# Kernel optimization log

Measured on AMD Instinct MI355X. Metric: run time of the kernel, lower is better.

The kernel has to match this reference:

```python
import jax, jax.numpy as jnp
import numpy as np

B, S, H = 2, 4096, 1024
WINDOW = 32


def setup_inputs() -> dict:
    key = jax.random.key(0)
    ks = jax.random.split(key, 10)
    s = 1.0 / np.sqrt(H)
    return {
        "hidden_states": jax.random.normal(ks[0], (B, S, H), dtype=jnp.float32),
        "Wq": jax.random.normal(ks[1], (H, H), dtype=jnp.float32) * s,
        "Wk": jax.random.normal(ks[2], (H, H), dtype=jnp.float32) * s,
        "Wv": jax.random.normal(ks[3], (H, H), dtype=jnp.float32) * s,
        "Wo": jax.random.normal(ks[4], (H, H), dtype=jnp.float32) * s,
        "ln_w": jnp.ones((H,), dtype=jnp.float32),
        "ln_b": jnp.zeros((H,), dtype=jnp.float32),
        "W1": jax.random.normal(ks[5], (H // 2, H), dtype=jnp.float32) * s,
        "b1": jnp.zeros((H // 2,), dtype=jnp.float32),
        "W2": jax.random.normal(ks[6], (H, H // 2), dtype=jnp.float32) * (1.0 / np.sqrt(H // 2)),
        "b2": jnp.zeros((H,), dtype=jnp.float32),
    }


def _layernorm(x, w, b, eps=1e-5):
    mu = jnp.mean(x, axis=-1, keepdims=True)
    var = jnp.var(x, axis=-1, keepdims=True)
    return (x - mu) * jax.lax.rsqrt(var + eps) * w + b


def reference(hidden_states, Wq, Wk, Wv, Wo, ln_w, ln_b, W1, b1, W2, b2):
    x = hidden_states  # [B,S,H]
    q = x @ Wq.T
    k = x @ Wk.T
    v = x @ Wv.T
    # banded causal mask: keep j<=i and j >= i-WINDOW+1
    i = jnp.arange(S)[:, None]
    j = jnp.arange(S)[None, :]
    local_mask = (j <= i) & (j >= i - WINDOW + 1)  # [S,S] bool
    scores = jnp.einsum('bqh,bkh->bqk', q, k) / np.sqrt(H)
    scores = jnp.where(local_mask[None], scores, -jnp.inf)
    probs = jax.nn.softmax(scores, axis=-1)
    attn_out = jnp.einsum('bqk,bkh->bqh', probs, v) @ Wo.T
    draft = x + attn_out
    h = _layernorm(draft, ln_w, ln_b)
    h = jax.nn.gelu(h @ W1.T + b1, approximate=False)
    adapter_out = h @ W2.T + b2
    return draft + adapter_out
```

## Files before the change

kernel.cpp:

```cpp
#include <hip/hip_runtime.h>
#include <stdint.h>

typedef unsigned short u16;
typedef __bf16 bfx8 __attribute__((ext_vector_type(8)));
typedef float f32x4 __attribute__((ext_vector_type(4)));

__device__ __forceinline__ u16 f2bf(float x) {
    unsigned int u = __float_as_uint(x);
    u += 0x7fffu + ((u >> 16) & 1u);
    return (u16)(u >> 16);
}
__device__ __forceinline__ float bf2f(u16 v) {
    return __uint_as_float(((unsigned)v) << 16);
}

__device__ __forceinline__ void async16(const void* g, void* l) {
    __builtin_amdgcn_global_load_lds(
        (const __attribute__((address_space(1))) unsigned int*)(uintptr_t)g,
        (__attribute__((address_space(3))) unsigned int*)(unsigned int)(uintptr_t)l,
        16, 0, 0);
}

#define S_BARRIER() asm volatile("s_barrier" ::: "memory")
#define WAIT_VM6() asm volatile("s_waitcnt vmcnt(6)" ::: "memory")
#define WAIT_VM5() asm volatile("s_waitcnt vmcnt(5)" ::: "memory")
#define WAIT_VM2() asm volatile("s_waitcnt vmcnt(2)" ::: "memory")
#define WAIT_VM0() asm volatile("s_waitcnt vmcnt(0)" ::: "memory")

struct CastArgs {
    const float* src[7];
    u16* dst[7];
    int nblk[7];
};
__global__ __launch_bounds__(256) void cast_all(CastArgs a) {
    int b = blockIdx.x, seg = 0;
    while (b >= a.nblk[seg]) { b -= a.nblk[seg]; ++seg; }
    int i = b * 256 + threadIdx.x;
    const float4* p = (const float4*)(a.src[seg] + (size_t)i * 8);
    float4 x = p[0], y = p[1];
    ushort4 o0, o1;
    o0.x = f2bf(x.x); o0.y = f2bf(x.y); o0.z = f2bf(x.z); o0.w = f2bf(x.w);
    o1.x = f2bf(y.x); o1.y = f2bf(y.y); o1.z = f2bf(y.z); o1.w = f2bf(y.w);
    ushort4* q = (ushort4*)(a.dst[seg] + (size_t)i * 8);
    q[0] = o0; q[1] = o1;
}

__global__ __launch_bounds__(512, 2)
void gemm_qkv2(const u16* __restrict__ A, const u16* __restrict__ Bw,
               u16* __restrict__ outq, u16* __restrict__ outk,
               u16* __restrict__ vt, int K) {
    __shared__ __align__(1024) unsigned char lds[131072];
    const int t = threadIdx.x;
    const int lane = t & 63, w = t >> 6;
    const int laneR = lane & 15, laneK = lane >> 4;
    const int wm = w >> 2, wn = w & 3;
    const int b = blockIdx.x;
    const int swz = (b & 7) * 48 + (b >> 3);
    const int row0 = (swz / 12) * 256;
    const int col0 = (swz % 12) * 256;
    const int nt = K >> 6;

    const u16* srcU[4][2];
    unsigned dstU[4][2];
#pragma unroll
    for (int u = 0; u < 4; ++u)
#pragma unroll
        for (int j = 0; j < 2; ++j) {
            int c = ((u & 1) ? 1024 : 0) + j * 512 + t;
            int row = c >> 3;
            int ko = (c & 7) ^ (row & 7);
            if (u < 2) srcU[u][j] = A + (size_t)(row0 + row) * K + ko * 8;
            else       srcU[u][j] = Bw + (size_t)(col0 + row) * K + ko * 8;
            dstU[u][j] = (u >= 2 ? 32768u : 0u) + (unsigned)c * 16u;
        }

#define QSTAGE(U, D, TK)                                                      \
    async16(srcU[U][0] + (TK) * 64, lds + (D) + dstU[U][0]);                  \
    async16(srcU[U][1] + (TK) * 64, lds + (D) + dstU[U][1]);

    f32x4 acc[8][4] = {};
    bfx8 af[4], bf[4];

#define QLDA(D, KS, H)                                                        \
    _Pragma("unroll") for (int m = 0; m < 4; ++m) {                           \
        int r = (H) * 128 + wm * 64 + m * 16 + laneR;                         \
        int ph = ((KS) * 4 + laneK) ^ (r & 7);                                \
        af[m] = *(const bfx8*)(lds + (D) + r * 128 + ph * 16);                \
    }
#define QLDB(D, KS)                                                           \
    _Pragma("unroll") for (int n = 0; n < 4; ++n) {                           \
        int rb = wn * 64 + n * 16 + laneR;                                    \
        int ph = ((KS) * 4 + laneK) ^ (rb & 7);                               \
        bf[n] = *(const bfx8*)(lds + (D) + 32768u + rb * 128 + ph * 16);      \
    }
#define QMFMA(H)                                                              \
    __builtin_amdgcn_s_setprio(1);                                            \
    _Pragma("unroll") for (int m = 0; m < 4; ++m)                             \
        _Pragma("unroll") for (int n = 0; n < 4; ++n)                         \
            acc[(H) * 4 + m][n] = __builtin_amdgcn_mfma_f32_16x16x32_bf16(    \
                af[m], bf[n], acc[(H) * 4 + m][n], 0, 0, 0);                  \
    __builtin_amdgcn_s_setprio(0);

    QSTAGE(0, 0u, 0) QSTAGE(2, 0u, 0) QSTAGE(3, 0u, 0) QSTAGE(1, 0u, 0)
    WAIT_VM2();
    S_BARRIER();

    for (int tk = 0; tk < nt - 1; ++tk) {
        const unsigned d = (unsigned)(tk & 1) * 65536u;
        const unsigned nd = d ^ 65536u;
        const int tn = tk + 1;
        QLDA(d, 0, 0) QLDB(d, 0) QSTAGE(0, nd, tn)
        S_BARRIER();
        QMFMA(0)
        WAIT_VM2();
        S_BARRIER();
        QLDA(d, 0, 1) QSTAGE(2, nd, tn)
        S_BARRIER();
        QMFMA(1)
        S_BARRIER();
        QLDA(d, 1, 0) QLDB(d, 1) QSTAGE(3, nd, tn)
        S_BARRIER();
        QMFMA(0)
        S_BARRIER();
        QLDA(d, 1, 1) QSTAGE(1, nd, tn)
        S_BARRIER();
        QMFMA(1)
        WAIT_VM2();
        S_BARRIER();
    }
    {
        const unsigned d = (unsigned)((nt - 1) & 1) * 65536u;
        QLDA(d, 0, 0) QLDB(d, 0)
        S_BARRIER();
        QMFMA(0)
        WAIT_VM0();
        S_BARRIER();
        QLDA(d, 0, 1)
        S_BARRIER();
        QMFMA(1)
        S_BARRIER();
        QLDA(d, 1, 0) QLDB(d, 1)
        S_BARRIER();
        QMFMA(0)
        S_BARRIER();
        QLDA(d, 1, 1)
        S_BARRIER();
        QMFMA(1)
    }

    const int colsec = col0 >> 10;
#pragma unroll
    for (int hi = 0; hi < 2; ++hi) {
#pragma unroll
        for (int mi = 0; mi < 4; ++mi) {
            const int gr0 = row0 + hi * 128 + wm * 64 + mi * 16 + laneK * 4;
#pragma unroll
            for (int n = 0; n < 4; ++n) {
                const int gc = col0 + wn * 64 + n * 16 + laneR;
                const f32x4 a4 = acc[hi * 4 + mi][n];
                if (colsec == 0) {
#pragma unroll
                    for (int r = 0; r < 4; ++r)
                        outq[(size_t)(gr0 + r) * 1024 + gc] = f2bf(a4[r]);
                } else if (colsec == 1) {
#pragma unroll
                    for (int r = 0; r < 4; ++r)
                        outk[(size_t)(gr0 + r) * 1024 + (gc - 1024)] = f2bf(a4[r]);
                } else {
                    ushort4 o4;
                    o4.x = f2bf(a4[0]); o4.y = f2bf(a4[1]);
                    o4.z = f2bf(a4[2]); o4.w = f2bf(a4[3]);
                    *(ushort4*)(vt + (((size_t)(gr0 >> 12)) * 1024 + (gc - 2048)) * 4096 +
                                (gr0 & 4095)) = o4;
                }
            }
        }
    }
#undef QSTAGE
#undef QLDA
#undef QLDB
#undef QMFMA
}

template <int EPI, int BNv>
__global__ __launch_bounds__(512, 2)
void gemm_ring(const u16* __restrict__ A, const u16* __restrict__ Bw,
               u16* __restrict__ outb, const float* __restrict__ bias,
               const u16* __restrict__ resb, u16* __restrict__ draftb,
               float* __restrict__ outf, int M, int N, int K, int ncol) {
    constexpr int NF = BNv / 32;
    constexpr int BU = BNv / 64;
    constexpr int TS = 32768 + BNv * 128;
    __shared__ __align__(1024) unsigned char lds[3 * TS];
    const int t = threadIdx.x;
    const int lane = t & 63, w = t >> 6;
    const int laneR = lane & 15, laneK = lane >> 4;
    const int wr = w >> 1, wc = w & 1;
    const int b = blockIdx.x;
    const int cpx = gridDim.x >> 3;
    const int swz = (b & 7) * cpx + (b >> 3);
    const int row0 = (swz / ncol) * 256, col0 = (swz % ncol) * BNv;
    const int nt = K >> 6;

    f32x4 acc[4][NF] = {};

    const u16* srcA[4];
    const u16* srcB[BU];
    unsigned dA[4], dB[BU];
#pragma unroll
    for (int i = 0; i < 4; ++i) {
        int li = i * 512 + t;
        int row = li >> 3, ko = li & 7;
        srcA[i] = A + (size_t)(row0 + row) * K + (ko ^ (row & 7)) * 8;
        dA[i] = li * 16;
    }
#pragma unroll
    for (int i = 0; i < BU; ++i) {
        int li = i * 512 + t;
        int row = li >> 3, ko = li & 7;
        srcB[i] = Bw + (size_t)(col0 + row) * K + (ko ^ (row & 7)) * 8;
        dB[i] = 32768 + li * 16;
    }

    auto stage = [&](int rb, int tk, int h) {
        unsigned char* base = lds + rb * TS;
        const int o = tk * 64;
        if (h == 0) {
            async16(srcA[0] + o, base + dA[0]);
            async16(srcA[1] + o, base + dA[1]);
            async16(srcB[0] + o, base + dB[0]);
        } else {
            async16(srcA[2] + o, base + dA[2]);
            async16(srcA[3] + o, base + dA[3]);
            if constexpr (BU == 2) async16(srcB[1] + o, base + dB[1]);
        }
    };

    stage(0, 0, 0); stage(0, 0, 1);
    stage(1, 1, 0); stage(1, 1, 1);
    if constexpr (BU == 2) { WAIT_VM6(); } else { WAIT_VM5(); }
    S_BARRIER();

    for (int tk = 0; tk < nt; ++tk) {
        unsigned char* bufA = lds + (tk % 3) * TS;
        unsigned char* bufB = bufA + 32768;
        const bool pf = (tk + 2 < nt);
        const int nb = (tk + 2) % 3;
#pragma unroll
        for (int ks = 0; ks < 2; ++ks) {
            bfx8 af[4], bf[NF];
#pragma unroll
            for (int m = 0; m < 4; ++m) {
                int r = wr * 64 + m * 16 + laneR;
                int phys = (ks * 4 + laneK) ^ (r & 7);
                af[m] = *(const bfx8*)(bufA + r * 128 + phys * 16);
            }
#pragma unroll
            for (int n = 0; n < NF; ++n) {
                int r = wc * (BNv / 2) + n * 16 + laneR;
                int phys = (ks * 4 + laneK) ^ (r & 7);
                bf[n] = *(const bfx8*)(bufB + r * 128 + phys * 16);
            }
            if (pf) stage(nb, tk + 2, ks);
            S_BARRIER();
            __builtin_amdgcn_s_setprio(1);
#pragma unroll
            for (int m = 0; m < 4; ++m)
#pragma unroll
                for (int n = 0; n < NF; ++n)
                    acc[m][n] = __builtin_amdgcn_mfma_f32_16x16x32_bf16(
                        af[m], bf[n], acc[m][n], 0, 0, 0);
            __builtin_amdgcn_s_setprio(0);
            if (ks == 1) {
                if (pf) {
                    if constexpr (BU == 2) { WAIT_VM6(); } else { WAIT_VM5(); }
                } else {
                    WAIT_VM0();
                }
            }
            S_BARRIER();
        }
    }

#pragma unroll
    for (int m = 0; m < 4; ++m) {
        const int gr0 = row0 + wr * 64 + m * 16 + laneK * 4;
#pragma unroll
        for (int n = 0; n < NF; ++n) {
            const int gc = col0 + wc * (BNv / 2) + n * 16 + laneR;
            if constexpr (EPI == 1) {
#pragma unroll
                for (int r = 0; r < 4; ++r) {
                    size_t idx = (size_t)(gr0 + r) * N + gc;
                    draftb[idx] = f2bf(bf2f(resb[idx]) + acc[m][n][r]);
                }
            } else if constexpr (EPI == 2) {
#pragma unroll
                for (int r = 0; r < 4; ++r) {
                    float xx = acc[m][n][r] + bias[gc];
                    outb[(size_t)(gr0 + r) * N + gc] =
                        f2bf(xx * 0.5f * (1.0f + erff(xx * 0.70710678118654752f)));
                }
            } else {
#pragma unroll
                for (int r = 0; r < 4; ++r) {
                    size_t idx = (size_t)(gr0 + r) * N + gc;
                    outf[idx] = bf2f(draftb[idx]) + acc[m][n][r] + bias[gc];
                }
            }
        }
    }
}

__global__ __launch_bounds__(256, 2)
void attn_kernel(const u16* __restrict__ Q, const u16* __restrict__ K,
                 const u16* __restrict__ vt, u16* __restrict__ O) {
    constexpr int H = 1024, S = 4096;
    const int t = threadIdx.x, lane = t & 63, w = t >> 6;
    const int laneR = lane & 15, laneK = lane >> 4;
    const int bb = blockIdx.x;
    const int tile = (bb & 7) * 32 + (bb >> 3);
    const int batch = tile >> 7;
    const int i0 = (tile & 127) * 32;
    const size_t base = (size_t)batch * S * H;

    __shared__ __align__(16) float S4[4][32][64];
    __shared__ __align__(16) u16 P[32][72];

    f32x4 sc[2][4] = {};
    for (int h = w * 256; h < w * 256 + 256; h += 32) {
        bfx8 qa[2];
#pragma unroll
        for (int m = 0; m < 2; ++m) {
            size_t row = (size_t)(i0 + m * 16 + laneR);
            qa[m] = *(const bfx8*)(Q + base + row * H + h + laneK * 8);
        }
        bfx8 kb[4];
#pragma unroll
        for (int n = 0; n < 4; ++n) {
            int j = i0 - 32 + n * 16 + laneR;
            int jc = j < 0 ? 0 : j;
            kb[n] = *(const bfx8*)(K + base + (size_t)jc * H + h + laneK * 8);
        }
#pragma unroll
        for (int m = 0; m < 2; ++m)
#pragma unroll
            for (int n = 0; n < 4; ++n)
                sc[m][n] = __builtin_amdgcn_mfma_f32_16x16x32_bf16(
                    qa[m], kb[n], sc[m][n], 0, 0, 0);
    }
#pragma unroll
    for (int m = 0; m < 2; ++m)
#pragma unroll
        for (int n = 0; n < 4; ++n)
#pragma unroll
            for (int r = 0; r < 4; ++r)
                S4[w][m * 16 + laneK * 4 + r][n * 16 + laneR] = sc[m][n][r];
    __syncthreads();

    {
        int q = t >> 3;
        int c0 = (t & 7) * 8;
        int lo = q + 1;
        if (32 - i0 > lo) lo = 32 - i0;
        int hi = q + 32;
        float vals[8];
        float mx = -1e30f;
#pragma unroll
        for (int c = 0; c < 8; ++c) {
            int cc = c0 + c;
            float v = (S4[0][q][cc] + S4[1][q][cc] + S4[2][q][cc] + S4[3][q][cc]) * 0.03125f;
            bool valid = (cc >= lo) && (cc <= hi);
            vals[c] = valid ? v : -1e30f;
            if (vals[c] > mx) mx = vals[c];
        }
#pragma unroll
        for (int d = 1; d < 8; d <<= 1) {
            float o = __shfl_xor(mx, d);
            if (o > mx) mx = o;
        }
        float sum = 0.f;
        float es[8];
#pragma unroll
        for (int c = 0; c < 8; ++c) {
            es[c] = (vals[c] > -1e29f) ? __expf(vals[c] - mx) : 0.f;
            sum += es[c];
        }
#pragma unroll
        for (int d = 1; d < 8; d <<= 1) sum += __shfl_xor(sum, d);
        float inv = 1.0f / sum;
#pragma unroll
        for (int c = 0; c < 8; ++c) P[q][c0 + c] = f2bf(es[c] * inv);
    }
    __syncthreads();

    for (int nc = 0; nc < 4; ++nc) {
        int ncol = w * 256 + nc * 64;
        f32x4 o[2][4] = {};
#pragma unroll
        for (int ks = 0; ks < 2; ++ks) {
            bfx8 pa[2];
#pragma unroll
            for (int m = 0; m < 2; ++m)
                pa[m] = *(const bfx8*)(&P[m * 16 + laneR][ks * 32 + laneK * 8]);
            int t0 = i0 - 32 + ks * 32 + laneK * 8;
            if (t0 < 0) t0 = 0;
#pragma unroll
            for (int n = 0; n < 4; ++n) {
                int c = ncol + n * 16 + laneR;
                bfx8 vb = *(const bfx8*)(vt + ((size_t)batch * 1024 + c) * 4096 + t0);
#pragma unroll
                for (int m = 0; m < 2; ++m)
                    o[m][n] = __builtin_amdgcn_mfma_f32_16x16x32_bf16(
                        pa[m], vb, o[m][n], 0, 0, 0);
            }
        }
#pragma unroll
        for (int m = 0; m < 2; ++m)
#pragma unroll
            for (int n = 0; n < 4; ++n)
#pragma unroll
                for (int r = 0; r < 4; ++r) {
                    size_t row = (size_t)(i0 + m * 16 + laneK * 4 + r);
                    O[base + row * H + ncol + n * 16 + laneR] = f2bf(o[m][n][r]);
                }
    }
}

__global__ __launch_bounds__(256)
void ln_kernel(const u16* __restrict__ xb, const float* __restrict__ gw,
               const float* __restrict__ gb, u16* __restrict__ out) {
    const int row = blockIdx.x, t = threadIdx.x;
    const ushort4 dv = ((const ushort4*)(xb + (size_t)row * 1024))[t];
    float4 v;
    v.x = bf2f(dv.x); v.y = bf2f(dv.y); v.z = bf2f(dv.z); v.w = bf2f(dv.w);
    float s = v.x + v.y + v.z + v.w;
    float s2 = v.x * v.x + v.y * v.y + v.z * v.z + v.w * v.w;
#pragma unroll
    for (int d = 1; d < 64; d <<= 1) {
        s += __shfl_xor(s, d);
        s2 += __shfl_xor(s2, d);
    }
    __shared__ float red[8];
    int lane = t & 63, wv = t >> 6;
    if (lane == 0) { red[wv] = s; red[4 + wv] = s2; }
    __syncthreads();
    float S1 = red[0] + red[1] + red[2] + red[3];
    float S2 = red[4] + red[5] + red[6] + red[7];
    float mu = S1 * (1.0f / 1024.0f);
    float var = S2 * (1.0f / 1024.0f) - mu * mu;
    float rstd = rsqrtf(var + 1e-5f);
    const float4 wv4 = ((const float4*)gw)[t];
    const float4 bv4 = ((const float4*)gb)[t];
    ushort4 o;
    o.x = f2bf((v.x - mu) * rstd * wv4.x + bv4.x);
    o.y = f2bf((v.y - mu) * rstd * wv4.y + bv4.y);
    o.z = f2bf((v.z - mu) * rstd * wv4.z + bv4.z);
    o.w = f2bf((v.w - mu) * rstd * wv4.w + bv4.w);
    ((ushort4*)(out + (size_t)row * 1024))[t] = o;
}

extern "C" void kernel_launch(void* const* d_in, const int* in_sizes, int n_in,
                              void* d_out, int out_size, void* d_ws, size_t ws_size,
                              hipStream_t stream) {
    const float* x   = (const float*)d_in[0];
    const float* Wq  = (const float*)d_in[1];
    const float* Wk  = (const float*)d_in[2];
    const float* Wv  = (const float*)d_in[3];
    const float* Wo  = (const float*)d_in[4];
    const float* lnw = (const float*)d_in[5];
    const float* lnb = (const float*)d_in[6];
    const float* W1  = (const float*)d_in[7];
    const float* b1  = (const float*)d_in[8];
    const float* W2  = (const float*)d_in[9];
    const float* b2  = (const float*)d_in[10];
    (void)in_sizes; (void)n_in; (void)out_size; (void)ws_size;

    const int M = 8192, H = 1024, Hh = 512;

    char* ws = (char*)d_ws;
    size_t off = 0;
    auto alloc = [&](size_t bytes) {
        char* p = ws + off;
        off += (bytes + 255) & ~(size_t)255;
        return p;
    };
    u16* Xb     = (u16*)alloc((size_t)M * H * 2);
    u16* Wqkvb  = (u16*)alloc((size_t)3 * H * H * 2);
    u16* Wob    = (u16*)alloc((size_t)H * H * 2);
    u16* W1b    = (u16*)alloc((size_t)Hh * H * 2);
    u16* W2b    = (u16*)alloc((size_t)H * Hh * 2);
    u16* Qb     = (u16*)alloc((size_t)M * H * 2);
    u16* Kb     = (u16*)alloc((size_t)M * H * 2);
    u16* Vt     = (u16*)alloc((size_t)M * H * 2);
    u16* draftb = (u16*)alloc((size_t)M * H * 2);
    u16* Attb   = (u16*)alloc((size_t)M * H * 2);
    u16* hlnb = Qb;
    u16* Gb   = Kb;
    float* outp = (float*)d_out;

    CastArgs ca;
    ca.src[0] = x;  ca.dst[0] = Xb;                        ca.nblk[0] = (M * H / 8) / 256;
    ca.src[1] = Wq; ca.dst[1] = Wqkvb;                     ca.nblk[1] = (H * H / 8) / 256;
    ca.src[2] = Wk; ca.dst[2] = Wqkvb + (size_t)H * H;     ca.nblk[2] = (H * H / 8) / 256;
    ca.src[3] = Wv; ca.dst[3] = Wqkvb + (size_t)2 * H * H; ca.nblk[3] = (H * H / 8) / 256;
    ca.src[4] = Wo; ca.dst[4] = Wob;                       ca.nblk[4] = (H * H / 8) / 256;
    ca.src[5] = W1; ca.dst[5] = W1b;                       ca.nblk[5] = (Hh * H / 8) / 256;
    ca.src[6] = W2; ca.dst[6] = W2b;                       ca.nblk[6] = (H * Hh / 8) / 256;
    int totblk = 0;
    for (int i = 0; i < 7; ++i) totblk += ca.nblk[i];
    cast_all<<<dim3(totblk), dim3(256), 0, stream>>>(ca);

    gemm_qkv2<<<dim3(384), dim3(512), 0, stream>>>(Xb, Wqkvb, Qb, Kb, Vt, H);

    attn_kernel<<<dim3(256), dim3(256), 0, stream>>>(Qb, Kb, Vt, Attb);

    gemm_ring<1, 128><<<dim3(256), dim3(512), 0, stream>>>(
        Attb, Wob, nullptr, nullptr, Xb, draftb, nullptr, M, H, H, 8);

    ln_kernel<<<dim3(M), dim3(256), 0, stream>>>(draftb, lnw, lnb, hlnb);

    gemm_ring<2, 64><<<dim3(256), dim3(512), 0, stream>>>(
        hlnb, W1b, Gb, b1, nullptr, nullptr, nullptr, M, Hh, H, 8);

    gemm_ring<3, 128><<<dim3(256), dim3(512), 0, stream>>>(
        Gb, W2b, nullptr, b2, nullptr, draftb, outp, M, H, Hh, 8);
}
```

Measured before the change: 167.9 us.

## Restructure QKV GEMM LDS layout into per-k-half slabs with deeper prefetch

The fused QKV GEMM now stores each 64-wide K tile in LDS as two 32-wide k-half slabs, using 64-byte rows and a new XOR swizzle, instead of one 128-byte-row tile. This lets the next tile's second half and the tile-after-next's first half be loaded into the buffer being consumed. Prefetch depth rises from about one tile to roughly one and a half, so global-load latency is hidden better. The warp row mapping also changes so each wave owns 128 contiguous rows. In exchange, wait-count bookkeeping and the tail handling become more intricate, and the new swizzle may change LDS bank-conflict behavior.

Result: slower. 173.3 us (+3.2%).

```diff
diff --git a/kernel.cpp b/kernel.cpp
--- a/kernel.cpp
+++ b/kernel.cpp
@@ -22,9 +22,10 @@
 }
 
 #define S_BARRIER() asm volatile("s_barrier" ::: "memory")
+#define WAIT_VM8() asm volatile("s_waitcnt vmcnt(8)" ::: "memory")
 #define WAIT_VM6() asm volatile("s_waitcnt vmcnt(6)" ::: "memory")
 #define WAIT_VM5() asm volatile("s_waitcnt vmcnt(5)" ::: "memory")
-#define WAIT_VM2() asm volatile("s_waitcnt vmcnt(2)" ::: "memory")
+#define WAIT_VM4() asm volatile("s_waitcnt vmcnt(4)" ::: "memory")
 #define WAIT_VM0() asm volatile("s_waitcnt vmcnt(0)" ::: "memory")
 
 struct CastArgs {
@@ -46,7 +47,7 @@
 }
 
 __global__ __launch_bounds__(512, 2)
-void gemm_qkv2(const u16* __restrict__ A, const u16* __restrict__ Bw,
+void gemm_qkv8(const u16* __restrict__ A, const u16* __restrict__ Bw,
                u16* __restrict__ outq, u16* __restrict__ outk,
                u16* __restrict__ vt, int K) {
     __shared__ __align__(1024) unsigned char lds[131072];
@@ -60,104 +61,93 @@
     const int col0 = (swz % 12) * 256;
     const int nt = K >> 6;
 
-    const u16* srcU[4][2];
-    unsigned dstU[4][2];
-#pragma unroll
-    for (int u = 0; u < 4; ++u)
-#pragma unroll
-        for (int j = 0; j < 2; ++j) {
-            int c = ((u & 1) ? 1024 : 0) + j * 512 + t;
-            int row = c >> 3;
-            int ko = (c & 7) ^ (row & 7);
-            if (u < 2) srcU[u][j] = A + (size_t)(row0 + row) * K + ko * 8;
-            else       srcU[u][j] = Bw + (size_t)(col0 + row) * K + ko * 8;
-            dstU[u][j] = (u >= 2 ? 32768u : 0u) + (unsigned)c * 16u;
-        }
-
-#define QSTAGE(U, D, TK)                                                      \
-    async16(srcU[U][0] + (TK) * 64, lds + (D) + dstU[U][0]);                  \
-    async16(srcU[U][1] + (TK) * 64, lds + (D) + dstU[U][1]);
+    const u16* pA[2];
+    const u16* pB[2];
+    unsigned dstc[2];
+#pragma unroll
+    for (int j = 0; j < 2; ++j) {
+        int c = j * 512 + t;
+        int row = c >> 2;
+        int ko = (c & 3) ^ ((row >> 1) & 3);
+        pA[j] = A + (size_t)(row0 + row) * K + ko * 8;
+        pB[j] = Bw + (size_t)(col0 + row) * K + ko * 8;
+        dstc[j] = (unsigned)c * 16u;
+    }
+
+#define SA8(D, KS, TK)                                                        \
+    async16(pA[0] + (TK) * 64 + (KS) * 32, lds + (D) + (KS) * 16384u + dstc[0]); \
+    async16(pA[1] + (TK) * 64 + (KS) * 32, lds + (D) + (KS) * 16384u + dstc[1]);
+#define SB8(D, KS, TK)                                                        \
+    async16(pB[0] + (TK) * 64 + (KS) * 32, lds + (D) + 32768u + (KS) * 16384u + dstc[0]); \
+    async16(pB[1] + (TK) * 64 + (KS) * 32, lds + (D) + 32768u + (KS) * 16384u + dstc[1]);
 
     f32x4 acc[8][4] = {};
     bfx8 af[4], bf[4];
 
-#define QLDA(D, KS, H)                                                        \
+#define LDA8(D, KS, Q)                                                        \
     _Pragma("unroll") for (int m = 0; m < 4; ++m) {                           \
-        int r = (H) * 128 + wm * 64 + m * 16 + laneR;                         \
-        int ph = ((KS) * 4 + laneK) ^ (r & 7);                                \
-        af[m] = *(const bfx8*)(lds + (D) + r * 128 + ph * 16);                \
-    }
-#define QLDB(D, KS)                                                           \
+        int r = wm * 128 + (Q) * 64 + m * 16 + laneR;                         \
+        af[m] = *(const bfx8*)(lds + (D) + (KS) * 16384u + r * 64 +           \
+                               ((laneK ^ ((r >> 1) & 3)) * 16));              \
+    }
+#define LDB8(D, KS)                                                           \
     _Pragma("unroll") for (int n = 0; n < 4; ++n) {                           \
-        int rb = wn * 64 + n * 16 + laneR;                                    \
-        int ph = ((KS) * 4 + laneK) ^ (rb & 7);                               \
-        bf[n] = *(const bfx8*)(lds + (D) + 32768u + rb * 128 + ph * 16);      \
-    }
-#define QMFMA(H)                                                              \
+        int r = wn * 64 + n * 16 + laneR;                                     \
+        bf[n] = *(const bfx8*)(lds + (D) + 32768u + (KS) * 16384u + r * 64 +  \
+                               ((laneK ^ ((r >> 1) & 3)) * 16));              \
+    }
+#define MF8(Q)                                                                \
     __builtin_amdgcn_s_setprio(1);                                            \
     _Pragma("unroll") for (int m = 0; m < 4; ++m)                             \
         _Pragma("unroll") for (int n = 0; n < 4; ++n)                         \
-            acc[(H) * 4 + m][n] = __builtin_amdgcn_mfma_f32_16x16x32_bf16(    \
-                af[m], bf[n], acc[(H) * 4 + m][n], 0, 0, 0);                  \
+            acc[(Q) * 4 + m][n] = __builtin_amdgcn_mfma_f32_16x16x32_bf16(    \
+                af[m], bf[n], acc[(Q) * 4 + m][n], 0, 0, 0);                  \
     __builtin_amdgcn_s_setprio(0);
 
-    QSTAGE(0, 0u, 0) QSTAGE(2, 0u, 0) QSTAGE(3, 0u, 0) QSTAGE(1, 0u, 0)
-    WAIT_VM2();
+    SA8(0u, 0, 0) SB8(0u, 0, 0) SA8(0u, 1, 0) SB8(0u, 1, 0)
+    SA8(65536u, 0, 1) SB8(65536u, 0, 1)
+    WAIT_VM8();
     S_BARRIER();
 
-    for (int tk = 0; tk < nt - 1; ++tk) {
+    for (int tk = 0; tk < nt; ++tk) {
         const unsigned d = (unsigned)(tk & 1) * 65536u;
         const unsigned nd = d ^ 65536u;
-        const int tn = tk + 1;
-        QLDA(d, 0, 0) QLDB(d, 0) QSTAGE(0, nd, tn)
-        S_BARRIER();
-        QMFMA(0)
-        WAIT_VM2();
-        S_BARRIER();
-        QLDA(d, 0, 1) QSTAGE(2, nd, tn)
-        S_BARRIER();
-        QMFMA(1)
-        S_BARRIER();
-        QLDA(d, 1, 0) QLDB(d, 1) QSTAGE(3, nd, tn)
-        S_BARRIER();
-        QMFMA(0)
-        S_BARRIER();
-        QLDA(d, 1, 1) QSTAGE(1, nd, tn)
-        S_BARRIER();
-        QMFMA(1)
-        WAIT_VM2();
-        S_BARRIER();
-    }
-    {
-        const unsigned d = (unsigned)((nt - 1) & 1) * 65536u;
-        QLDA(d, 0, 0) QLDB(d, 0)
-        S_BARRIER();
-        QMFMA(0)
-        WAIT_VM0();
-        S_BARRIER();
-        QLDA(d, 0, 1)
-        S_BARRIER();
-        QMFMA(1)
-        S_BARRIER();
-        QLDA(d, 1, 0) QLDB(d, 1)
-        S_BARRIER();
-        QMFMA(0)
-        S_BARRIER();
-        QLDA(d, 1, 1)
-        S_BARRIER();
-        QMFMA(1)
+        const bool s1 = (tk + 1 < nt), s2 = (tk + 2 < nt);
+        LDA8(d, 0, 0) LDB8(d, 0)
+        if (s1) { SA8(nd, 1, tk + 1) }
+        S_BARRIER();
+        MF8(0)
+        S_BARRIER();
+        LDA8(d, 0, 1)
+        if (s1) { SB8(nd, 1, tk + 1) }
+        S_BARRIER();
+        MF8(1)
+        if (s1) { WAIT_VM6(); } else { WAIT_VM0(); }
+        S_BARRIER();
+        LDA8(d, 1, 0) LDB8(d, 1)
+        if (s2) { SA8(d, 0, tk + 2) }
+        S_BARRIER();
+        MF8(0)
+        S_BARRIER();
+        LDA8(d, 1, 1)
+        if (s2) { SB8(d, 0, tk + 2) }
+        S_BARRIER();
+        MF8(1)
+        if (s2) { WAIT_VM6(); }
+        else if (s1) { WAIT_VM4(); }
+        S_BARRIER();
     }
 
     const int colsec = col0 >> 10;
 #pragma unroll
-    for (int hi = 0; hi < 2; ++hi) {
+    for (int q = 0; q < 2; ++q) {
 #pragma unroll
         for (int mi = 0; mi < 4; ++mi) {
-            const int gr0 = row0 + hi * 128 + wm * 64 + mi * 16 + laneK * 4;
+            const int gr0 = row0 + wm * 128 + q * 64 + mi * 16 + laneK * 4;
 #pragma unroll
             for (int n = 0; n < 4; ++n) {
                 const int gc = col0 + wn * 64 + n * 16 + laneR;
-                const f32x4 a4 = acc[hi * 4 + mi][n];
+                const f32x4 a4 = acc[q * 4 + mi][n];
                 if (colsec == 0) {
 #pragma unroll
                     for (int r = 0; r < 4; ++r)
@@ -176,10 +166,11 @@
             }
         }
     }
-#undef QSTAGE
-#undef QLDA
-#undef QLDB
-#undef QMFMA
+#undef SA8
+#undef SB8
+#undef LDA8
+#undef LDB8
+#undef MF8
 }
 
 template <int EPI, int BNv>
@@ -511,7 +502,7 @@
     for (int i = 0; i < 7; ++i) totblk += ca.nblk[i];
     cast_all<<<dim3(totblk), dim3(256), 0, stream>>>(ca);
 
-    gemm_qkv2<<<dim3(384), dim3(512), 0, stream>>>(Xb, Wqkvb, Qb, Kb, Vt, H);
+    gemm_qkv8<<<dim3(384), dim3(512), 0, stream>>>(Xb, Wqkvb, Qb, Kb, Vt, H);
 
     attn_kernel<<<dim3(256), dim3(256), 0, stream>>>(Qb, Kb, Vt, Attb);
 
```
